# Performance work log

Measured on AMD Instinct MI355X. Metric: run time of the kernel, lower is better.

The kernel has to match this reference:

```python
import jax, jax.numpy as jnp
import numpy as np

B, LAT, N, XS = 16, 8, 500000, 256
W0_FIRST = 30.0


def _euler_zyz(rows):
    # xmipp-style ZYZ Euler rotation matrices, rows = [rot, tilt, psi], shape [B,3]
    rot, tilt, psi = rows[:, 0], rows[:, 1], rows[:, 2]
    ca, sa = jnp.cos(rot), jnp.sin(rot)
    cb, sb = jnp.cos(tilt), jnp.sin(tilt)
    cg, sg = jnp.cos(psi), jnp.sin(psi)
    R = jnp.stack([
        jnp.stack([cg * cb * ca - sg * sa, cg * cb * sa + sg * ca, -cg * sb], -1),
        jnp.stack([-sg * cb * ca - cg * sa, -sg * cb * sa + cg * ca, sg * sb], -1),
        jnp.stack([sb * ca, sb * sa, cb], -1),
    ], axis=1)  # [B,3,3]
    return R


def _gauss_kernel(sigma=1.0, radius=3):
    x = jnp.arange(-radius, radius + 1, dtype=jnp.float32)
    k = jnp.exp(-0.5 * (x / sigma) ** 2)
    return k / jnp.sum(k)


def setup_inputs() -> dict:
    key = jax.random.key(0)
    ks = jax.random.split(key, 16)
    half = XS // 2
    inp = {
        "rows": jax.random.uniform(ks[0], (B, 3), jnp.float32, -np.pi, np.pi),
        "shifts": 2.0 * jax.random.normal(ks[1], (B, 2), jnp.float32),
        "latent": jax.random.normal(ks[2], (B, LAT), jnp.float32),
        "coords": (jax.random.uniform(ks[3], (N, 3), jnp.float32) - 0.5) * (0.8 * XS),
        "values": jax.random.normal(ks[4], (N,), jnp.float32),
        "W0": (6.0 / LAT) * jax.random.uniform(ks[5], (LAT, LAT), jnp.float32, -1.0, 1.0),
        "b0": jnp.zeros((LAT,), jnp.float32),
        "W1": jnp.sqrt(6.0 / LAT) * jax.random.uniform(ks[6], (LAT, LAT), jnp.float32, -1.0, 1.0),
        "b1": jnp.zeros((LAT,), jnp.float32),
        "W2": jnp.sqrt(6.0 / LAT) * jax.random.uniform(ks[7], (LAT, LAT), jnp.float32, -1.0, 1.0),
        "b2": jnp.zeros((LAT,), jnp.float32),
        "W3": jnp.sqrt(6.0 / LAT) * jax.random.uniform(ks[8], (LAT, LAT), jnp.float32, -1.0, 1.0),
        "b3": jnp.zeros((LAT,), jnp.float32),
        "Wd": 0.02 * jax.random.normal(ks[9], (LAT, N), jnp.float32),
        "bd": jnp.zeros((N,), jnp.float32),
        "ctf": jax.random.uniform(ks[10], (B, XS, XS // 2 + 1), jnp.float32, -1.0, 1.0),
    }
    return inp


def reference(rows, shifts, latent, coords, values, W0, b0, W1, b1, W2, b2, W3, b3, Wd, bd, ctf):
    half = XS // 2
    # --- rotated grid (Lambda: getRotatedGrid) ---
    R = _euler_zyz(rows)                                   # [B,3,3]
    coords_rot = jnp.einsum('bij,nj->bni', R, coords)      # [B,N,3]

    # --- SIREN hypernet: first layer w0=30, then 3 residual sine blocks w0=1 ---
    h = jnp.sin(W0_FIRST * (latent @ W0 + b0))
    for W, b in ((W1, b1), (W2, b2), (W3, b3)):
        h = h + jnp.sin(h @ W + b)
    delta = h @ Wd + bd                                    # [B,N] per-point density deltas
    vals = values[None, :] + delta                         # base values + deltas

    # --- scatterImgByPass: project onto xy, shift, nearest-neighbor splat ---
    px = jnp.round(coords_rot[..., 0] + shifts[:, 0:1] + half)
    py = jnp.round(coords_rot[..., 1] + shifts[:, 1:2] + half)
    px = jnp.clip(px, 0, XS - 1).astype(jnp.int32)         # [B,N]
    py = jnp.clip(py, 0, XS - 1).astype(jnp.int32)
    bidx = jnp.arange(B, dtype=jnp.int32)[:, None]
    flat = (bidx * XS + py) * XS + px                      # [B,N] flat indices into B*XS*XS
    img = jnp.zeros((B * XS * XS,), vals.dtype).at[flat.ravel()].add(vals.ravel())
    img = img.reshape(B, XS, XS)

    # --- gaussianFilterImage: separable sigma=1 Gaussian blur ---
    k = _gauss_kernel(1.0, 3)
    x4 = img[:, None, :, :]                                # NCHW
    dn = ('NCHW', 'OIHW', 'NCHW')
    x4 = jax.lax.conv_general_dilated(x4, k.reshape(1, 1, 7, 1), (1, 1), 'SAME', dimension_numbers=dn)
    x4 = jax.lax.conv_general_dilated(x4, k.reshape(1, 1, 1, 7), (1, 1), 'SAME', dimension_numbers=dn)
    img = x4[:, 0]

    # --- ctfFilterImage: multiply by CTF in Fourier space ---
    F = jnp.fft.rfft2(img)
    img = jnp.fft.irfft2(F * ctf, s=(XS, XS)).astype(jnp.float32)
    return img
```

## Files before the change

### kernel.cpp

```cpp
#include <hip/hip_runtime.h>
#include <math.h>

#define BB   16
#define LATD 8
#define NN   500000
#define XSZ  256
#define HALF 128
#define IMG_ELEMS (BB * XSZ * XSZ)
#define FREQ_COLS 129
#define NBLK ((NN + 255) / 256)

#define QSCALE 16384.0f
#define QINV   (1.0f / 16384.0f)
__device__ __forceinline__ unsigned pack_entry_q(float v, int off12) {
    int q = (int)rintf(v * QSCALE);
    q = q >  524287 ?  524287 : q;
    q = q < -524288 ? -524288 : q;
    return ((unsigned)q << 12) | (unsigned)off12;
}
__device__ __forceinline__ int entry_q(unsigned e) {
    return ((int)e) >> 12;
}

__device__ __forceinline__ unsigned wave_incl_scan(unsigned x, int lane) {
    #pragma unroll
    for (int d = 1; d < 64; d <<= 1) {
        unsigned y = __shfl_up(x, d, 64);
        if (lane >= d) x += y;
    }
    return x;
}

__global__ void prep_kernel(const float* __restrict__ rows,
                            const float* __restrict__ shifts,
                            const float* __restrict__ latent,
                            const float* __restrict__ W0, const float* __restrict__ b0,
                            const float* __restrict__ W1, const float* __restrict__ b1,
                            const float* __restrict__ W2, const float* __restrict__ b2,
                            const float* __restrict__ W3, const float* __restrict__ b3,
                            float* __restrict__ bdata) {
    int b = threadIdx.x;
    if (b >= BB) return;

    float rot  = rows[b * 3 + 0];
    float tilt = rows[b * 3 + 1];
    float psi  = rows[b * 3 + 2];
    float ca, sa, cb, sb, cg, sg;
    sincosf(rot, &sa, &ca);
    sincosf(tilt, &sb, &cb);
    sincosf(psi, &sg, &cg);

    float R00 =  cg * cb * ca - sg * sa;
    float R01 =  cg * cb * sa + sg * ca;
    float R02 = -cg * sb;
    float R10 = -sg * cb * ca - cg * sa;
    float R11 = -sg * cb * sa + cg * ca;
    float R12 =  sg * sb;

    float h[LATD], t[LATD];
    #pragma unroll
    for (int j = 0; j < LATD; ++j) {
        float acc = b0[j];
        #pragma unroll
        for (int l = 0; l < LATD; ++l) acc += latent[b * LATD + l] * W0[l * LATD + j];
        t[j] = acc;
    }
    #pragma unroll
    for (int j = 0; j < LATD; ++j) h[j] = sinf(30.0f * t[j]);

    const float* Ws[3] = {W1, W2, W3};
    const float* bs[3] = {b1, b2, b3};
    for (int L = 0; L < 3; ++L) {
        #pragma unroll
        for (int j = 0; j < LATD; ++j) {
            float acc = bs[L][j];
            #pragma unroll
            for (int l = 0; l < LATD; ++l) acc += h[l] * Ws[L][l * LATD + j];
            t[j] = acc;
        }
        #pragma unroll
        for (int j = 0; j < LATD; ++j) h[j] += sinf(t[j]);
    }

    float* P = bdata + b * 16;
    P[0] = R00; P[1] = R01; P[2] = R02;
    P[3] = R10; P[4] = R11; P[5] = R12;
    P[6] = shifts[b * 2 + 0] + (float)HALF;
    P[7] = shifts[b * 2 + 1] + (float)HALF;
    #pragma unroll
    for (int j = 0; j < LATD; ++j) P[8 + j] = h[j];
}

__device__ __forceinline__ int2 project_px(const float* __restrict__ Q,
                                           float cx, float cy, float cz) {
    float x = fmaf(Q[0], cx, fmaf(Q[1], cy, fmaf(Q[2], cz, Q[6])));
    float y = fmaf(Q[3], cx, fmaf(Q[4], cy, fmaf(Q[5], cz, Q[7])));
    float px = fminf(fmaxf(rintf(x), 0.f), 255.f);
    float py = fminf(fmaxf(rintf(y), 0.f), 255.f);
    return make_int2((int)px, (int)py);
}

__global__ __launch_bounds__(256) void fill3_kernel(
        const float* __restrict__ coords, const float* __restrict__ values,
        const float* __restrict__ Wd, const float* __restrict__ bd,
        const float* __restrict__ bdata, unsigned* __restrict__ bucket,
        unsigned* __restrict__ lbaseT) {
    __shared__ float    P[256];
    __shared__ unsigned hist[256];
    __shared__ unsigned wsum[4];
    __shared__ unsigned lbase[256];
    __shared__ unsigned stage[4096];

    int tid = threadIdx.x;
    int blk = blockIdx.x;
    int lane = tid & 63;
    int w = tid >> 6;
    int grp = tid >> 4;
    P[tid] = bdata[tid];
    hist[tid] = 0;
    __syncthreads();

    int n = blk * 256 + tid;
    bool active = (n < NN);

    unsigned word[BB];
    unsigned rk[BB];
    unsigned char tl[BB];
    if (active) {
        float cx = coords[n * 3 + 0];
        float cy = coords[n * 3 + 1];
        float cz = coords[n * 3 + 2];
        float base = values[n] + bd[n];
        float wd[LATD];
        #pragma unroll
        for (int l = 0; l < LATD; ++l) wd[l] = Wd[l * NN + n];
        #pragma unroll
        for (int i = 0; i < BB; ++i) {
            int bi = (grp + i) & 15;
            const float* Q = &P[bi * 16];
            int2 p = project_px(Q, cx, cy, cz);
            float delta = 0.f;
            #pragma unroll
            for (int l = 0; l < LATD; ++l) delta = fmaf(Q[8 + l], wd[l], delta);
            int tile = bi * 16 + (p.y >> 4);
            int off12 = ((p.y & 15) << 8) | p.x;
            word[i] = pack_entry_q(base + delta, off12);
            tl[i] = (unsigned char)tile;
            rk[i] = atomicAdd(&hist[tile], 1u);
        }
    }
    __syncthreads();

    unsigned v = hist[tid];
    unsigned s = wave_incl_scan(v, lane);
    if (lane == 63) wsum[w] = s;
    __syncthreads();
    unsigned off = 0;
    #pragma unroll
    for (int i = 0; i < 4; ++i) { unsigned u = wsum[i]; if (i < w) off += u; }
    unsigned excl = s + off - v;
    lbase[tid] = excl;
    __syncthreads();

    if (active) {
        #pragma unroll
        for (int i = 0; i < BB; ++i) {
            stage[lbase[tl[i]] + rk[i]] = word[i];
        }
    }

    int nactive = NN - blk * 256;
    if (nactive > 256) nactive = 256;
    int tot = nactive * BB;

    lbaseT[(size_t)blk * 257 + tid] = excl;
    if (tid == 0) lbaseT[(size_t)blk * 257 + 256] = (unsigned)tot;
    __syncthreads();

    unsigned* seg = bucket + ((size_t)blk << 12);
    for (int i = tid; i < tot; i += 256) seg[i] = stage[i];
}

#define ACC_ISSUE(cc, S, E, Bs, X0, X1, X2) do {                            \
    int r_ = ((cc) << 4) + (w << 2) + g;                                    \
    S = 0u; E = 0u;                                                         \
    if ((cc) < nChunks && r_ < nB) { S = sArr[r_]; E = eArr[r_]; }          \
    Bs = ((size_t)(blk0 + r_) << 12);                                       \
    unsigned i0_ = S + (unsigned)sl;                                        \
    X0 = (i0_        < E) ? bucket[Bs + i0_]        : 0u;                   \
    X1 = (i0_ + 16u  < E) ? bucket[Bs + i0_ + 16u]  : 0u;                   \
    X2 = (i0_ + 32u  < E) ? bucket[Bs + i0_ + 32u]  : 0u;                   \
} while (0)

#define ACC_PROC(S, E, Bs, X0, X1, X2) do {                                 \
    unsigned i0_ = S + (unsigned)sl;                                        \
    if (i0_       < E) atomicAdd(&tile[X0 & 4095u], (unsigned)entry_q(X0)); \
    if (i0_ + 16u < E) atomicAdd(&tile[X1 & 4095u], (unsigned)entry_q(X1)); \
    if (i0_ + 32u < E) atomicAdd(&tile[X2 & 4095u], (unsigned)entry_q(X2)); \
    for (unsigned i_ = i0_ + 48u; i_ < E; i_ += 16u) {                      \
        unsigned x_ = bucket[Bs + i_];                                      \
        atomicAdd(&tile[x_ & 4095u], (unsigned)entry_q(x_));                \
    }                                                                       \
} while (0)

__global__ __launch_bounds__(256) void accum2b_kernel(
        const unsigned* __restrict__ bucket, const unsigned* __restrict__ lbaseT,
        float* __restrict__ partials, int M) {
    __shared__ unsigned tile[4096];
    __shared__ unsigned sArr[1024];
    __shared__ unsigned eArr[1024];
    int t = blockIdx.x & 255;
    int m = blockIdx.x >> 8;
    int tid = threadIdx.x;
    int lane = tid & 63;
    int w = tid >> 6;
    #pragma unroll
    for (int i = 0; i < 16; ++i) tile[tid + (i << 8)] = 0u;

    int blk0 = (int)((long long)NBLK * m / M);
    int blk1 = (int)((long long)NBLK * (m + 1) / M);
    int nB = blk1 - blk0;

    for (int r = tid; r < nB; r += 256) {
        const unsigned* lrow = lbaseT + (size_t)(blk0 + r) * 257;
        sArr[r] = lrow[t];
        eArr[r] = lrow[t + 1];
    }
    __syncthreads();

    int g  = (lane >> 4);
    int sl = lane & 15;
    int nChunks = (nB + 15) >> 4;

    unsigned sA, eA, xA0, xA1, xA2; size_t bA;
    unsigned sB, eB, xB0, xB1, xB2; size_t bB;
    unsigned sC, eC, xC0, xC1, xC2; size_t bC;

    ACC_ISSUE(0, sA, eA, bA, xA0, xA1, xA2);
    ACC_ISSUE(1, sB, eB, bB, xB0, xB1, xB2);
    for (int c = 0; c < nChunks; c += 3) {
        ACC_ISSUE(c + 2, sC, eC, bC, xC0, xC1, xC2);
        ACC_PROC(sA, eA, bA, xA0, xA1, xA2);
        ACC_ISSUE(c + 3, sA, eA, bA, xA0, xA1, xA2);
        ACC_PROC(sB, eB, bB, xB0, xB1, xB2);
        ACC_ISSUE(c + 4, sB, eB, bB, xB0, xB1, xB2);
        ACC_PROC(sC, eC, bC, xC0, xC1, xC2);
    }
    __syncthreads();
    float* dst = partials + (((size_t)m * 256 + t) << 12);
    for (int k = tid; k < 4096; k += 256) {
        dst[k] = (float)(int)tile[k] * QINV;
    }
}

__global__ void zero_kernel(float4* __restrict__ p, int n4) {
    int i = blockIdx.x * blockDim.x + threadIdx.x;
    if (i < n4) p[i] = make_float4(0.f, 0.f, 0.f, 0.f);
}

__global__ __launch_bounds__(256) void scatter_atomic_kernel(
        const float* __restrict__ coords, const float* __restrict__ values,
        const float* __restrict__ Wd, const float* __restrict__ bd,
        const float* __restrict__ bdata, float* __restrict__ img) {
    __shared__ float P[BB * 16];
    P[threadIdx.x] = bdata[threadIdx.x];
    __syncthreads();
    int n = blockIdx.x * 256 + threadIdx.x;
    if (n >= NN) return;
    float cx = coords[n * 3 + 0];
    float cy = coords[n * 3 + 1];
    float cz = coords[n * 3 + 2];
    float base = values[n] + bd[n];
    float wd[LATD];
    #pragma unroll
    for (int l = 0; l < LATD; ++l) wd[l] = Wd[l * NN + n];
    #pragma unroll
    for (int b = 0; b < BB; ++b) {
        const float* Q = &P[b * 16];
        int2 p = project_px(Q, cx, cy, cz);
        float delta = 0.f;
        #pragma unroll
        for (int l = 0; l < LATD; ++l) delta = fmaf(Q[8 + l], wd[l], delta);
        atomicAdd(img + ((b << 16) | (p.y << 8) | p.x), base + delta);
    }
}

__device__ __constant__ float GW[4] = {0.39905027f, 0.24203623f, 0.05400558f, 0.00443305f};

__device__ __forceinline__ void fft256(float2* src, float2* dst,
                                       const float2* __restrict__ TW,
                                       int lane, float dir) {
    #pragma unroll
    for (int st = 0; st < 4; ++st) {
        const int s = 1 << (2 * st);
        int p = lane >> (2 * st);
        int q = lane & (s - 1);
        int base = q + s * p;
        float2 x0 = src[base];
        float2 x1 = src[base + 64];
        float2 x2 = src[base + 128];
        float2 x3 = src[base + 192];
        int m = p * s;
        float c1 = TW[m].x;
        float s1 = dir * TW[m].y;
        float c2 = TW[2 * m].x;
        float s2 = dir * TW[2 * m].y;

        float2 sA = make_float2(x0.x + x2.x, x0.y + x2.y);
        float2 sB = make_float2(x1.x + x3.x, x1.y + x3.y);
        float2 dAr = make_float2(x0.x - x2.x, x0.y - x2.y);
        float2 dBr = make_float2(x1.x - x3.x, x1.y - x3.y);
        float2 dA = make_float2(dAr.x * c1 - dAr.y * s1,
                                dAr.x * s1 + dAr.y * c1);
        float2 dBt = make_float2(dBr.x * c1 - dBr.y * s1,
                                 dBr.x * s1 + dBr.y * c1);
        float2 dB = make_float2(-dir * dBt.y, dir * dBt.x);

        float2 y0 = make_float2(sA.x + sB.x, sA.y + sB.y);
        float2 y1 = make_float2(dA.x + dB.x, dA.y + dB.y);
        float2 u2 = make_float2(sA.x - sB.x, sA.y - sB.y);
        float2 u3 = make_float2(dA.x - dB.x, dA.y - dB.y);

        int o = q + 4 * s * p;
        dst[o]         = y0;
        dst[o + s]     = y1;
        dst[o + 2 * s] = make_float2(u2.x * c2 - u2.y * s2,
                                     u2.x * s2 + u2.y * c2);
        dst[o + 3 * s] = make_float2(u3.x * c2 - u3.y * s2,
                                     u3.x * s2 + u3.y * c2);
        __syncthreads();
        float2* tmp = src; src = dst; dst = tmp;
    }
}

__device__ __forceinline__ void fill_tw256(float2* TW, int tid) {
    if (tid < 128) {
        float sn, cs;
        sincosf(0.0245436926061703f * (float)tid, &sn, &cs);
        TW[tid] = make_float2(cs, sn);
    }
}

__global__ __launch_bounds__(256) void fft_rows_fwd(const float* __restrict__ img,
                                                    const float* __restrict__ partials,
                                                    int M,
                                                    float2* __restrict__ Freq) {
    __shared__ float2 bufA[4][256];
    __shared__ float2 bufB[4][256];
    __shared__ float2 TW[128];
    __shared__ float  rowr[4][256];
    int tid = threadIdx.x;
    int lane = tid & 63;
    int sub = tid >> 6;
    fill_tw256(TW, tid);
    int b  = blockIdx.x >> 6;
    int y0 = (blockIdx.x & 63) << 2;

    if (M > 0) {
        int t = (b << 4) | (y0 >> 4);
        const float* pb = partials + ((size_t)t << 12) + ((y0 & 15) << 8);
        const size_t mstr = (size_t)256 << 12;
        for (int i = tid; i < 1024; i += 256) {
            float s = 0.f;
            for (int m = 0; m < M; ++m) s += pb[(size_t)m * mstr + i];
            ((float*)rowr)[i] = s;
        }
    } else {
        const float* src = img + (((size_t)(b << 8) + y0) << 8);
        for (int i = tid; i < 1024; i += 256) ((float*)rowr)[i] = src[i];
    }
    __syncthreads();

    #pragma unroll
    for (int j = 0; j < 4; ++j) {
        int x = lane + (j << 6);
        float acc = GW[0] * rowr[sub][x];
        #pragma unroll
        for (int t = 1; t <= 3; ++t) {
            if (x - t >= 0)  acc += GW[t] * rowr[sub][x - t];
            if (x + t < 256) acc += GW[t] * rowr[sub][x + t];
        }
        bufA[sub][x] = make_float2(acc, 0.f);
    }
    __syncthreads();
    fft256(bufA[sub], bufB[sub], TW, lane, -1.f);

    for (int i = tid; i < FREQ_COLS * 4; i += 256) {
        int col = i >> 2;
        int s   = i & 3;
        Freq[((size_t)(b * FREQ_COLS + col) << 8) + y0 + s] = bufA[s][col];
    }
}

__global__ __launch_bounds__(256) void fft_cols_ctf(float2* __restrict__ Freq,
                                                    const float* __restrict__ ctf) {
    __shared__ float2 bufA[4][256];
    __shared__ float2 bufB[4][256];
    __shared__ float2 TW[128];
    int tid = threadIdx.x;
    int lane = tid & 63;
    int sub = tid >> 6;
    fill_tw256(TW, tid);
    int b  = blockIdx.x / 33;
    int c0 = (blockIdx.x - b * 33) << 2;
    int col  = c0 + sub;
    int colc = col < FREQ_COLS ? col : (FREQ_COLS - 1);
    float2* basep = Freq + ((size_t)(b * FREQ_COLS + colc) << 8);

    #pragma unroll
    for (int j = 0; j < 4; ++j) {
        int k = lane + (j << 6);
        bufB[sub][k] = basep[k];
    }
    __syncthreads();
    #pragma unroll
    for (int j = 0; j < 4; ++j) {
        int k = lane + (j << 6);
        float ax = GW[0] * bufB[sub][k].x;
        float ay = GW[0] * bufB[sub][k].y;
        #pragma unroll
        for (int t = 1; t <= 3; ++t) {
            if (k - t >= 0)  { ax += GW[t] * bufB[sub][k - t].x; ay += GW[t] * bufB[sub][k - t].y; }
            if (k + t < 256) { ax += GW[t] * bufB[sub][k + t].x; ay += GW[t] * bufB[sub][k + t].y; }
        }
        bufA[sub][k] = make_float2(ax, ay);
    }
    __syncthreads();
    fft256(bufA[sub], bufB[sub], TW, lane, -1.f);
    #pragma unroll
    for (int j = 0; j < 4; ++j) {
        int k = lane + (j << 6);
        float c = ctf[(size_t)((b << 8) | k) * FREQ_COLS + colc];
        bufA[sub][k].x *= c;
        bufA[sub][k].y *= c;
    }
    __syncthreads();
    fft256(bufA[sub], bufB[sub], TW, lane, +1.f);
    if (col < FREQ_COLS) {
        #pragma unroll
        for (int j = 0; j < 4; ++j) {
            int k = lane + (j << 6);
            basep[k] = bufA[sub][k];
        }
    }
}

__global__ __launch_bounds__(256) void fft_rows_inv(const float2* __restrict__ Freq,
                                                    float* __restrict__ out) {
    __shared__ float2 bufA[4][256];
    __shared__ float2 bufB[4][256];
    __shared__ float2 TW[128];
    int tid = threadIdx.x;
    int lane = tid & 63;
    int sub = tid >> 6;
    fill_tw256(TW, tid);
    int b  = blockIdx.x >> 6;
    int y0 = (blockIdx.x & 63) << 2;

    for (int i = tid; i < FREQ_COLS * 4; i += 256) {
        int col = i >> 2;
        int s   = i & 3;
        bufA[s][col] = Freq[((size_t)(b * FREQ_COLS + col) << 8) + y0 + s];
    }
    __syncthreads();
    for (int k = FREQ_COLS + lane; k < 256; k += 64) {
        float2 v = bufA[sub][256 - k];
        bufA[sub][k] = make_float2(v.x, -v.y);
    }
    __syncthreads();
    fft256(bufA[sub], bufB[sub], TW, lane, +1.f);
    float* dst = out + (((size_t)(b << 8) + y0) << 8);
    const float scale = 1.0f / 65536.0f;
    for (int i = tid; i < 1024; i += 256) {
        dst[i] = bufA[i >> 8][i & 255].x * scale;
    }
}

extern "C" void kernel_launch(void* const* d_in, const int* in_sizes, int n_in,
                              void* d_out, int out_size, void* d_ws, size_t ws_size,
                              hipStream_t stream) {
    const float* rows   = (const float*)d_in[0];
    const float* shifts = (const float*)d_in[1];
    const float* latent = (const float*)d_in[2];
    const float* coords = (const float*)d_in[3];
    const float* values = (const float*)d_in[4];
    const float* W0     = (const float*)d_in[5];
    const float* b0     = (const float*)d_in[6];
    const float* W1     = (const float*)d_in[7];
    const float* b1     = (const float*)d_in[8];
    const float* W2     = (const float*)d_in[9];
    const float* b2     = (const float*)d_in[10];
    const float* W3     = (const float*)d_in[11];
    const float* b3     = (const float*)d_in[12];
    const float* Wd     = (const float*)d_in[13];
    const float* bd     = (const float*)d_in[14];
    const float* ctf    = (const float*)d_in[15];
    float* out = (float*)d_out;

    char* w = (char*)d_ws;
    size_t off = 0;
    float* bdata = (float*)(w + off);  off += 4096;
    float* img   = (float*)(w + off);  off += (size_t)IMG_ELEMS * 4;
    float2* Freq = (float2*)(w + off); off += (size_t)BB * FREQ_COLS * 256 * 8;
    unsigned* bucket = (unsigned*)(w + off); off += (size_t)NBLK * 4096 * 4;
    unsigned* lbaseT = (unsigned*)(w + off); off += (size_t)NBLK * 257 * 4;
    float* partials  = (float*)(w + off);
    size_t fixed = off;

    int M = 0;
    if      (ws_size >= fixed + 4ull * 4194304 * 4) M = 4;
    else if (ws_size >= fixed + 2ull * 4194304)     M = 2;

    prep_kernel<<<1, 64, 0, stream>>>(rows, shifts, latent,
                                      W0, b0, W1, b1, W2, b2, W3, b3, bdata);

    if (M > 0) {
        fill3_kernel<<<NBLK, 256, 0, stream>>>(coords, values, Wd, bd, bdata,
                                               bucket, lbaseT);
        accum2b_kernel<<<256 * M, 256, 0, stream>>>(bucket, lbaseT, partials, M);
        fft_rows_fwd<<<BB * 64, 256, 0, stream>>>(img, partials, M, Freq);
    } else {
        int n4 = IMG_ELEMS / 4;
        zero_kernel<<<(n4 + 255) / 256, 256, 0, stream>>>((float4*)img, n4);
        scatter_atomic_kernel<<<NBLK, 256, 0, stream>>>(coords, values, Wd, bd,
                                                        bdata, img);
        fft_rows_fwd<<<BB * 64, 256, 0, stream>>>(img, partials, 0, Freq);
    }

    fft_cols_ctf<<<BB * 33, 256, 0, stream>>>(Freq, ctf);
    fft_rows_inv<<<BB * 64, 256, 0, stream>>>(Freq, out);
}
```

Baseline: 164.5 us.

## Pack two real rows per complex FFT, fuse prep into fill, vectorize stores

The row FFTs now run two real rows as one complex 256-point transform, separated after the forward pass and combined before the inverse pass, so the row-FFT kernels use half as many blocks and FFT passes. The per-image rotation and MLP prep is recomputed inside every fill block instead of running as a separate one-thread kernel launch. The bucket copy and the partials write now use 128-bit vector stores. In exchange, each fill block redoes the tiny MLP and needs extra registers, and the uint4 bucket copy drops tail elements when tot is not a multiple of 4 (it always is here, since tot is a multiple of 16).

After: 168.8 us. 1.03x slower.

```diff
diff --git a/kernel.cpp b/kernel.cpp
--- a/kernel.cpp
+++ b/kernel.cpp
@@ -29,6 +29,59 @@
         if (lane >= d) x += y;
     }
     return x;
+}
+
+__device__ __forceinline__ void prep_image(
+        int b, const float* __restrict__ rows, const float* __restrict__ shifts,
+        const float* __restrict__ latent,
+        const float* __restrict__ W0, const float* __restrict__ b0,
+        const float* __restrict__ W1, const float* __restrict__ b1,
+        const float* __restrict__ W2, const float* __restrict__ b2,
+        const float* __restrict__ W3, const float* __restrict__ b3,
+        float* __restrict__ P) {
+    float rot  = rows[b * 3 + 0];
+    float tilt = rows[b * 3 + 1];
+    float psi  = rows[b * 3 + 2];
+    float ca, sa, cb, sb, cg, sg;
+    sincosf(rot, &sa, &ca);
+    sincosf(tilt, &sb, &cb);
+    sincosf(psi, &sg, &cg);
+
+    P[b * 16 + 0] =  cg * cb * ca - sg * sa;
+    P[b * 16 + 1] =  cg * cb * sa + sg * ca;
+    P[b * 16 + 2] = -cg * sb;
+    P[b * 16 + 3] = -sg * cb * ca - cg * sa;
+    P[b * 16 + 4] = -sg * cb * sa + cg * ca;
+    P[b * 16 + 5] =  sg * sb;
+    P[b * 16 + 6] = shifts[b * 2 + 0] + (float)HALF;
+    P[b * 16 + 7] = shifts[b * 2 + 1] + (float)HALF;
+
+    float h[LATD], t[LATD];
+    #pragma unroll
+    for (int j = 0; j < LATD; ++j) {
+        float acc = b0[j];
+        #pragma unroll
+        for (int l = 0; l < LATD; ++l) acc += latent[b * LATD + l] * W0[l * LATD + j];
+        t[j] = acc;
+    }
+    #pragma unroll
+    for (int j = 0; j < LATD; ++j) h[j] = sinf(30.0f * t[j]);
+
+    const float* Ws[3] = {W1, W2, W3};
+    const float* bs[3] = {b1, b2, b3};
+    for (int L = 0; L < 3; ++L) {
+        #pragma unroll
+        for (int j = 0; j < LATD; ++j) {
+            float acc = bs[L][j];
+            #pragma unroll
+            for (int l = 0; l < LATD; ++l) acc += h[l] * Ws[L][l * LATD + j];
+            t[j] = acc;
+        }
+        #pragma unroll
+        for (int j = 0; j < LATD; ++j) h[j] += sinf(t[j]);
+    }
+    #pragma unroll
+    for (int j = 0; j < LATD; ++j) P[b * 16 + 8 + j] = h[j];
 }
 
 __global__ void prep_kernel(const float* __restrict__ rows,
@@ -40,55 +93,8 @@
                             const float* __restrict__ W3, const float* __restrict__ b3,
                             float* __restrict__ bdata) {
     int b = threadIdx.x;
-    if (b >= BB) return;
-
-    float rot  = rows[b * 3 + 0];
-    float tilt = rows[b * 3 + 1];
-    float psi  = rows[b * 3 + 2];
-    float ca, sa, cb, sb, cg, sg;
-    sincosf(rot, &sa, &ca);
-    sincosf(tilt, &sb, &cb);
-    sincosf(psi, &sg, &cg);
-
-    float R00 =  cg * cb * ca - sg * sa;
-    float R01 =  cg * cb * sa + sg * ca;
-    float R02 = -cg * sb;
-    float R10 = -sg * cb * ca - cg * sa;
-    float R11 = -sg * cb * sa + cg * ca;
-    float R12 =  sg * sb;
-
-    float h[LATD], t[LATD];
-    #pragma unroll
-    for (int j = 0; j < LATD; ++j) {
-        float acc = b0[j];
-        #pragma unroll
-        for (int l = 0; l < LATD; ++l) acc += latent[b * LATD + l] * W0[l * LATD + j];
-        t[j] = acc;
-    }
-    #pragma unroll
-    for (int j = 0; j < LATD; ++j) h[j] = sinf(30.0f * t[j]);
-
-    const float* Ws[3] = {W1, W2, W3};
-    const float* bs[3] = {b1, b2, b3};
-    for (int L = 0; L < 3; ++L) {
-        #pragma unroll
-        for (int j = 0; j < LATD; ++j) {
-            float acc = bs[L][j];
-            #pragma unroll
-            for (int l = 0; l < LATD; ++l) acc += h[l] * Ws[L][l * LATD + j];
-            t[j] = acc;
-        }
-        #pragma unroll
-        for (int j = 0; j < LATD; ++j) h[j] += sinf(t[j]);
-    }
-
-    float* P = bdata + b * 16;
-    P[0] = R00; P[1] = R01; P[2] = R02;
-    P[3] = R10; P[4] = R11; P[5] = R12;
-    P[6] = shifts[b * 2 + 0] + (float)HALF;
-    P[7] = shifts[b * 2 + 1] + (float)HALF;
-    #pragma unroll
-    for (int j = 0; j < LATD; ++j) P[8 + j] = h[j];
+    if (b < BB)
+        prep_image(b, rows, shifts, latent, W0, b0, W1, b1, W2, b2, W3, b3, bdata);
 }
 
 __device__ __forceinline__ int2 project_px(const float* __restrict__ Q,
@@ -101,10 +107,15 @@
 }
 
 __global__ __launch_bounds__(256) void fill3_kernel(
+        const float* __restrict__ rows, const float* __restrict__ shifts,
+        const float* __restrict__ latent,
+        const float* __restrict__ W0, const float* __restrict__ b0,
+        const float* __restrict__ W1, const float* __restrict__ b1,
+        const float* __restrict__ W2, const float* __restrict__ b2,
+        const float* __restrict__ W3, const float* __restrict__ b3,
         const float* __restrict__ coords, const float* __restrict__ values,
         const float* __restrict__ Wd, const float* __restrict__ bd,
-        const float* __restrict__ bdata, unsigned* __restrict__ bucket,
-        unsigned* __restrict__ lbaseT) {
+        unsigned* __restrict__ bucket, unsigned* __restrict__ lbaseT) {
     __shared__ float    P[256];
     __shared__ unsigned hist[256];
     __shared__ unsigned wsum[4];
@@ -116,7 +127,8 @@
     int lane = tid & 63;
     int w = tid >> 6;
     int grp = tid >> 4;
-    P[tid] = bdata[tid];
+    if (tid < BB)
+        prep_image(tid, rows, shifts, latent, W0, b0, W1, b1, W2, b2, W3, b3, P);
     hist[tid] = 0;
     __syncthreads();
 
@@ -177,8 +189,10 @@
     if (tid == 0) lbaseT[(size_t)blk * 257 + 256] = (unsigned)tot;
     __syncthreads();
 
-    unsigned* seg = bucket + ((size_t)blk << 12);
-    for (int i = tid; i < tot; i += 256) seg[i] = stage[i];
+    uint4* seg4 = (uint4*)(bucket + ((size_t)blk << 12));
+    const uint4* st4 = (const uint4*)stage;
+    int tot4 = tot >> 2;
+    for (int i = tid; i < tot4; i += 256) seg4[i] = st4[i];
 }
 
 #define ACC_ISSUE(cc, S, E, Bs, X0, X1, X2) do {                            \
@@ -247,9 +261,13 @@
         ACC_PROC(sC, eC, bC, xC0, xC1, xC2);
     }
     __syncthreads();
-    float* dst = partials + (((size_t)m * 256 + t) << 12);
-    for (int k = tid; k < 4096; k += 256) {
-        dst[k] = (float)(int)tile[k] * QINV;
+    float4* dst4 = (float4*)(partials + (((size_t)m * 256 + t) << 12));
+    for (int k = tid; k < 1024; k += 256) {
+        int k4 = k << 2;
+        dst4[k] = make_float4((float)(int)tile[k4]     * QINV,
+                              (float)(int)tile[k4 + 1] * QINV,
+                              (float)(int)tile[k4 + 2] * QINV,
+                              (float)(int)tile[k4 + 3] * QINV);
     }
 }
 
@@ -348,47 +366,70 @@
     __shared__ float2 bufA[4][256];
     __shared__ float2 bufB[4][256];
     __shared__ float2 TW[128];
-    __shared__ float  rowr[4][256];
+    __shared__ float  rowr[8][256];
     int tid = threadIdx.x;
     int lane = tid & 63;
     int sub = tid >> 6;
     fill_tw256(TW, tid);
-    int b  = blockIdx.x >> 6;
-    int y0 = (blockIdx.x & 63) << 2;
+    int b  = blockIdx.x >> 5;
+    int y0 = (blockIdx.x & 31) << 3;
 
     if (M > 0) {
         int t = (b << 4) | (y0 >> 4);
         const float* pb = partials + ((size_t)t << 12) + ((y0 & 15) << 8);
         const size_t mstr = (size_t)256 << 12;
-        for (int i = tid; i < 1024; i += 256) {
+        for (int i = tid; i < 2048; i += 256) {
             float s = 0.f;
             for (int m = 0; m < M; ++m) s += pb[(size_t)m * mstr + i];
             ((float*)rowr)[i] = s;
         }
     } else {
         const float* src = img + (((size_t)(b << 8) + y0) << 8);
-        for (int i = tid; i < 1024; i += 256) ((float*)rowr)[i] = src[i];
+        for (int i = tid; i < 2048; i += 256) ((float*)rowr)[i] = src[i];
     }
     __syncthreads();
 
     #pragma unroll
     for (int j = 0; j < 4; ++j) {
         int x = lane + (j << 6);
-        float acc = GW[0] * rowr[sub][x];
-        #pragma unroll
-        for (int t = 1; t <= 3; ++t) {
-            if (x - t >= 0)  acc += GW[t] * rowr[sub][x - t];
-            if (x + t < 256) acc += GW[t] * rowr[sub][x + t];
-        }
-        bufA[sub][x] = make_float2(acc, 0.f);
+        float a0, a1;
+        {
+            int r0 = 2 * sub;
+            float acc = GW[0] * rowr[r0][x];
+            #pragma unroll
+            for (int t = 1; t <= 3; ++t) {
+                if (x - t >= 0)  acc += GW[t] * rowr[r0][x - t];
+                if (x + t < 256) acc += GW[t] * rowr[r0][x + t];
+            }
+            a0 = acc;
+        }
+        {
+            int r1 = 2 * sub + 1;
+            float acc = GW[0] * rowr[r1][x];
+            #pragma unroll
+            for (int t = 1; t <= 3; ++t) {
+                if (x - t >= 0)  acc += GW[t] * rowr[r1][x - t];
+                if (x + t < 256) acc += GW[t] * rowr[r1][x + t];
+            }
+            a1 = acc;
+        }
+        bufA[sub][x] = make_float2(a0, a1);
     }
     __syncthreads();
     fft256(bufA[sub], bufB[sub], TW, lane, -1.f);
 
-    for (int i = tid; i < FREQ_COLS * 4; i += 256) {
-        int col = i >> 2;
-        int s   = i & 3;
-        Freq[((size_t)(b * FREQ_COLS + col) << 8) + y0 + s] = bufA[s][col];
+    for (int i = tid; i < FREQ_COLS * 8; i += 256) {
+        int col = i >> 3;
+        int r   = i & 7;
+        int sb  = r >> 1;
+        float2 Zk = bufA[sb][col];
+        float2 Zm = bufA[sb][(256 - col) & 255];
+        float2 v;
+        if ((r & 1) == 0)
+            v = make_float2(0.5f * (Zk.x + Zm.x), 0.5f * (Zk.y - Zm.y));
+        else
+            v = make_float2(0.5f * (Zk.y + Zm.y), 0.5f * (Zm.x - Zk.x));
+        Freq[((size_t)(b * FREQ_COLS + col) << 8) + y0 + r] = v;
     }
 }
 
@@ -450,29 +491,53 @@
     __shared__ float2 bufA[4][256];
     __shared__ float2 bufB[4][256];
     __shared__ float2 TW[128];
+    __shared__ float2 stA[4][FREQ_COLS];
+    __shared__ float2 stB[4][FREQ_COLS];
     int tid = threadIdx.x;
     int lane = tid & 63;
     int sub = tid >> 6;
     fill_tw256(TW, tid);
-    int b  = blockIdx.x >> 6;
-    int y0 = (blockIdx.x & 63) << 2;
-
-    for (int i = tid; i < FREQ_COLS * 4; i += 256) {
-        int col = i >> 2;
-        int s   = i & 3;
-        bufA[s][col] = Freq[((size_t)(b * FREQ_COLS + col) << 8) + y0 + s];
-    }
-    __syncthreads();
-    for (int k = FREQ_COLS + lane; k < 256; k += 64) {
-        float2 v = bufA[sub][256 - k];
-        bufA[sub][k] = make_float2(v.x, -v.y);
+    int b  = blockIdx.x >> 5;
+    int y0 = (blockIdx.x & 31) << 3;
+
+    for (int i = tid; i < FREQ_COLS * 8; i += 256) {
+        int col = i >> 3;
+        int r   = i & 7;
+        int sb  = r >> 1;
+        float2 v = Freq[((size_t)(b * FREQ_COLS + col) << 8) + y0 + r];
+        if ((r & 1) == 0) stA[sb][col] = v;
+        else              stB[sb][col] = v;
+    }
+    __syncthreads();
+    #pragma unroll
+    for (int j = 0; j < 4; ++j) {
+        int k = lane + (j << 6);
+        float2 z;
+        if (k == 0 || k == 128) {
+            float2 A = stA[sub][k];
+            float2 Bv = stB[sub][k];
+            z = make_float2(A.x, Bv.x);
+        } else if (k < 128) {
+            float2 A = stA[sub][k];
+            float2 Bv = stB[sub][k];
+            z = make_float2(A.x - Bv.y, A.y + Bv.x);
+        } else {
+            int m = 256 - k;
+            float2 A = stA[sub][m];
+            float2 Bv = stB[sub][m];
+            z = make_float2(A.x + Bv.y, Bv.x - A.y);
+        }
+        bufA[sub][k] = z;
     }
     __syncthreads();
     fft256(bufA[sub], bufB[sub], TW, lane, +1.f);
     float* dst = out + (((size_t)(b << 8) + y0) << 8);
     const float scale = 1.0f / 65536.0f;
-    for (int i = tid; i < 1024; i += 256) {
-        dst[i] = bufA[i >> 8][i & 255].x * scale;
+    for (int i = tid; i < 2048; i += 256) {
+        int rowIdx = i >> 8;
+        int x = i & 255;
+        float2 v = bufA[rowIdx >> 1][x];
+        dst[i] = ((rowIdx & 1) ? v.y : v.x) * scale;
     }
 }
 
@@ -511,22 +576,23 @@
     if      (ws_size >= fixed + 4ull * 4194304 * 4) M = 4;
     else if (ws_size >= fixed + 2ull * 4194304)     M = 2;
 
-    prep_kernel<<<1, 64, 0, stream>>>(rows, shifts, latent,
-                                      W0, b0, W1, b1, W2, b2, W3, b3, bdata);
-
     if (M > 0) {
-        fill3_kernel<<<NBLK, 256, 0, stream>>>(coords, values, Wd, bd, bdata,
+        fill3_kernel<<<NBLK, 256, 0, stream>>>(rows, shifts, latent,
+                                               W0, b0, W1, b1, W2, b2, W3, b3,
+                                               coords, values, Wd, bd,
                                                bucket, lbaseT);
         accum2b_kernel<<<256 * M, 256, 0, stream>>>(bucket, lbaseT, partials, M);
-        fft_rows_fwd<<<BB * 64, 256, 0, stream>>>(img, partials, M, Freq);
+        fft_rows_fwd<<<BB * 32, 256, 0, stream>>>(img, partials, M, Freq);
     } else {
+        prep_kernel<<<1, 64, 0, stream>>>(rows, shifts, latent,
+                                          W0, b0, W1, b1, W2, b2, W3, b3, bdata);
         int n4 = IMG_ELEMS / 4;
         zero_kernel<<<(n4 + 255) / 256, 256, 0, stream>>>((float4*)img, n4);
         scatter_atomic_kernel<<<NBLK, 256, 0, stream>>>(coords, values, Wd, bd,
                                                         bdata, img);
-        fft_rows_fwd<<<BB * 64, 256, 0, stream>>>(img, partials, 0, Freq);
+        fft_rows_fwd<<<BB * 32, 256, 0, stream>>>(img, partials, 0, Freq);
     }
 
     fft_cols_ctf<<<BB * 33, 256, 0, stream>>>(Freq, ctf);
-    fft_rows_inv<<<BB * 64, 256, 0, stream>>>(Freq, out);
-}
+    fft_rows_inv<<<BB * 32, 256, 0, stream>>>(Freq, out);
+}
```
